# Kernel optimization log

Hardware: AMD Instinct MI355X
Metric: run time of the kernel (lower is better)

Reference implementation:

```python
import jax, jax.numpy as jnp
import numpy as np

NUM_SPECIES = 10


def setup_inputs() -> dict:
    key = jax.random.key(0)
    ks = jax.random.split(key, 8)
    n, k, d = 1024, 64, 9          # nodes, channels (num_features), irrep dim (0e+1o+2e)
    A1, A2, A3 = 3, 8, 18          # CG path counts per correlation order 1,2,3
    A = A1 + A2 + A3
    x = jax.random.normal(ks[0], (n, k, d), jnp.float32)
    counts = np.full((NUM_SPECIES,), n // NUM_SPECIES, dtype=np.int32)
    counts[0] += n - counts.sum()  # exact partition of the n nodes by species
    species_counts = jnp.asarray(counts, jnp.int32)
    w = jax.random.normal(ks[1], (NUM_SPECIES, A, k), jnp.float32) * 0.5
    projection = jax.random.normal(ks[2], (A, A), jnp.float32) / jnp.sqrt(A)
    U1 = jax.random.normal(ks[3], (d, d, A1), jnp.float32) * 0.3            # [o, i1, a]
    U2 = jax.random.normal(ks[4], (d, d, d, A2), jnp.float32) * 0.3         # [o, i1, i2, a]
    U3 = jax.random.normal(ks[5], (d, d, d, d, A3), jnp.float32) * 0.3      # [o, i1, i2, i3, a]
    return {"x": x, "species_counts": species_counts, "w": w,
            "projection": projection, "U1": U1, "U2": U2, "U3": U3}


def reference(x, species_counts, w, projection, U1, U2, U3):
    # x: [n, k, d] node features (channels k, irrep dim d)
    e = w.shape[0]
    n = x.shape[0]
    A1, A2 = U1.shape[-1], U2.shape[-1]
    # sorted per-node species index, exactly as in the original module
    species_idx = jnp.repeat(jnp.arange(e), species_counts, total_repeat_length=n)
    onehot = jax.nn.one_hot(species_idx, e, dtype=x.dtype)            # [n, e]
    # project raw weights onto the coupling-path basis: 'zau,ab->zbu'
    wp = jnp.einsum('zak,ab->zbk', w, projection)                     # [e, A, k]
    w1, w2, w3 = wp[:, :A1], wp[:, A1:A1 + A2], wp[:, A1 + A2:]
    # --- correlation 3 term, Horner scheme (MACE order) ---
    # fold species weights into the basis tensor (small: e*d^4*k)
    Uw3 = jnp.einsum('oijla,eak->eoijlk', U3, w3)                     # [e,o,i,j,l,k]
    # species-masked features (small: n*e*k*d) to avoid a per-node d^4 gather
    xe = jnp.einsum('ne,nkl->nekl', onehot, x)                        # [n,e,k,d]
    out = jnp.einsum('eoijlk,nekl->nkoij', Uw3, xe)                   # [n,k,o,i,j]
    # --- correlation 2 term ---
    c2 = jnp.einsum('oija,eak,ne->nkoij', U2, w2, onehot)             # [n,k,o,i,j]
    out = jnp.einsum('nkoij,nkj->nkoi', out + c2, x)                  # contract i2
    # --- correlation 1 term ---
    c1 = jnp.einsum('oia,eak,ne->nkoi', U1, w1, onehot)               # [n,k,o,i]
    out = jnp.einsum('nkoi,nki->nko', out + c1, x)                    # contract i1
    return out                                                        # [n, k, d_out] = n m i
```

## Files before the change

kernel.cpp:

```cpp
#include <hip/hip_runtime.h>

constexpr int N_ = 1024, K_ = 64, D_ = 9, E_ = 10;
constexpr int A1_ = 3, A2_ = 8, A3_ = 18, A_ = 29;
constexpr int NP2 = 45;
constexpr int NP3 = 165;

constexpr int OFF_WP  = 0;
constexpr int OFF_U3S = OFF_WP  + E_*A_*K_;
constexpr int OFF_U2S = OFF_U3S + NP3*D_*A3_;
constexpr int OFF_S3  = OFF_U2S + NP2*D_*A2_;
constexpr int OFF_S2  = OFF_S3  + E_*K_*NP3*D_;
constexpr int OFF_C1  = OFF_S2  + E_*K_*NP2*D_;
constexpr int WS_FLOATS = OFF_C1 + E_*K_*D_*D_;

__global__ void prep_kernel(const float* __restrict__ w,
                            const float* __restrict__ proj,
                            const float* __restrict__ U2,
                            const float* __restrict__ U3,
                            float* __restrict__ ws) {
  const int WP_N  = E_*A_*K_;
  const int U3S_N = NP3*D_*A3_;
  const int U2S_N = NP2*D_*A2_;
  int idx = blockIdx.x * blockDim.x + threadIdx.x;
  if (idx < WP_N) {
    int e = idx / (A_*K_); int r = idx % (A_*K_); int b = r / K_; int k = r % K_;
    float acc = 0.f;
    for (int a = 0; a < A_; ++a)
      acc = fmaf(w[(e*A_ + a)*K_ + k], proj[a*A_ + b], acc);
    ws[OFF_WP + idx] = acc;
  } else if (idx < WP_N + U3S_N) {
    int id = idx - WP_N;
    int t = id / (D_*A3_); int r = id % (D_*A3_); int o = r / A3_; int m = r % A3_;
    int ti = 0, tj = 0, tl = 0, c = 0;
    for (int a = 0; a < D_; ++a)
      for (int b = a; b < D_; ++b)
        for (int g = b; g < D_; ++g) { if (c == t) { ti = a; tj = b; tl = g; } ++c; }
    auto u3 = [&](int a, int b, int g) {
      return U3[(((o*D_ + a)*D_ + b)*D_ + g)*A3_ + m];
    };
    float s;
    if (ti == tj && tj == tl)      s = u3(ti, ti, ti);
    else if (ti == tj)             s = u3(ti, ti, tl) + u3(ti, tl, ti) + u3(tl, ti, ti);
    else if (tj == tl)             s = u3(ti, tj, tj) + u3(tj, ti, tj) + u3(tj, tj, ti);
    else                           s = u3(ti, tj, tl) + u3(ti, tl, tj) + u3(tj, ti, tl)
                                     + u3(tj, tl, ti) + u3(tl, ti, tj) + u3(tl, tj, ti);
    ws[OFF_U3S + id] = s;
  } else if (idx < WP_N + U3S_N + U2S_N) {
    int id = idx - WP_N - U3S_N;
    int p = id / (D_*A2_); int r = id % (D_*A2_); int o = r / A2_; int m = r % A2_;
    int pi = 0, pj = 0, c = 0;
    for (int a = 0; a < D_; ++a)
      for (int b = a; b < D_; ++b) { if (c == p) { pi = a; pj = b; } ++c; }
    float s = U2[((o*D_ + pi)*D_ + pj)*A2_ + m];
    if (pi != pj) s += U2[((o*D_ + pj)*D_ + pi)*A2_ + m];
    ws[OFF_U2S + id] = s;
  }
}

__global__ void weights_kernel(const float* __restrict__ U1,
                               float* __restrict__ ws) {
  int ek = blockIdx.x;
  int e = ek / K_, k = ek % K_;
  __shared__ float wpk[A_];
  if (threadIdx.x < A_)
    wpk[threadIdx.x] = ws[OFF_WP + (e*A_ + threadIdx.x)*K_ + k];
  __syncthreads();
  const float* u3s = ws + OFF_U3S;
  const float* u2s = ws + OFF_U2S;
  float* s3 = ws + OFF_S3 + ek*(NP3*D_);
  float* s2 = ws + OFF_S2 + ek*(NP2*D_);
  float* c1 = ws + OFF_C1 + ek*(D_*D_);
  const int TOT = NP3*D_ + NP2*D_ + D_*D_;
  for (int idx = threadIdx.x; idx < TOT; idx += blockDim.x) {
    if (idx < NP3*D_) {
      int t = idx / D_, o = idx % D_;
      float acc = 0.f;
      #pragma unroll
      for (int m = 0; m < A3_; ++m)
        acc = fmaf(u3s[(t*D_ + o)*A3_ + m], wpk[A1_ + A2_ + m], acc);
      s3[t*D_ + o] = acc;
    } else if (idx < NP3*D_ + NP2*D_) {
      int id = idx - NP3*D_;
      int p = id / D_, o = id % D_;
      float acc = 0.f;
      #pragma unroll
      for (int m = 0; m < A2_; ++m)
        acc = fmaf(u2s[(p*D_ + o)*A2_ + m], wpk[A1_ + m], acc);
      s2[p*D_ + o] = acc;
    } else {
      int id = idx - NP3*D_ - NP2*D_;
      int i = id / D_, o = id % D_;
      float acc = 0.f;
      #pragma unroll
      for (int m = 0; m < A1_; ++m)
        acc = fmaf(U1[(o*D_ + i)*A1_ + m], wpk[m], acc);
      c1[i*D_ + o] = acc;
    }
  }
}

__global__ __launch_bounds__(128) void main_kernel(const float* __restrict__ x,
                                                   const int* __restrict__ counts,
                                                   const float* __restrict__ ws,
                                                   float* __restrict__ out) {
  int ek = blockIdx.x;
  int e = ek / K_, k = ek % K_;
  int start = 0;
  for (int s = 0; s < e; ++s) start += counts[s];
  int cnt = counts[e];
  int tid = threadIdx.x;
  bool active = tid < cnt;
  int n = start + tid;
  int nc = active ? n : start;
  const float* xp = x + (nc*K_ + k)*D_;
  float xv[D_];
  #pragma unroll
  for (int l = 0; l < D_; ++l) xv[l] = xp[l];

  const float* s3 = ws + OFF_S3 + ek*(NP3*D_);
  const float* s2 = ws + OFF_S2 + ek*(NP2*D_);
  const float* c1 = ws + OFF_C1 + ek*(D_*D_);

  float acc[D_];
  #pragma unroll
  for (int o = 0; o < D_; ++o) acc[o] = 0.f;

  int t = 0, p = 0;
  #pragma unroll
  for (int i = 0; i < D_; ++i) {
    float xi = xv[i];
    #pragma unroll
    for (int o = 0; o < D_; ++o) acc[o] = fmaf(c1[i*D_ + o], xi, acc[o]);
    #pragma unroll
    for (int j = i; j < D_; ++j) {
      float xij = xi * xv[j];
      #pragma unroll
      for (int o = 0; o < D_; ++o) acc[o] = fmaf(s2[p*D_ + o], xij, acc[o]);
      ++p;
      #pragma unroll
      for (int l = j; l < D_; ++l) {
        float xijl = xij * xv[l];
        #pragma unroll
        for (int o = 0; o < D_; ++o) acc[o] = fmaf(s3[t*D_ + o], xijl, acc[o]);
        ++t;
      }
    }
  }

  if (active) {
    float* op = out + (n*K_ + k)*D_;
    #pragma unroll
    for (int o = 0; o < D_; ++o) op[o] = acc[o];
  }
}

extern "C" void kernel_launch(void* const* d_in, const int* in_sizes, int n_in,
                              void* d_out, int out_size, void* d_ws, size_t ws_size,
                              hipStream_t stream) {
  const float* x     = (const float*)d_in[0];
  const int*   cnts  = (const int*)  d_in[1];
  const float* w     = (const float*)d_in[2];
  const float* proj  = (const float*)d_in[3];
  const float* U1    = (const float*)d_in[4];
  const float* U2    = (const float*)d_in[5];
  const float* U3    = (const float*)d_in[6];
  float* out = (float*)d_out;
  float* ws  = (float*)d_ws;

  const int PREP_N = E_*A_*K_ + NP3*D_*A3_ + NP2*D_*A2_;
  int prep_blocks = (PREP_N + 255) / 256;
  prep_kernel<<<prep_blocks, 256, 0, stream>>>(w, proj, U2, U3, ws);
  weights_kernel<<<E_*K_, 256, 0, stream>>>(U1, ws);
  main_kernel<<<E_*K_, 128, 0, stream>>>(x, cnts, ws, out);
}
```

Baseline: 106.7 us.

## Fuse per-species weight folding into main kernel and transpose U tables

Merges the weights kernel into the main compute kernel, so each block first builds its own (species, channel) coefficient table into a per-block workspace slice, then runs the polynomial evaluation from it after a block barrier. The symmetrized U2/U3 tables are stored path-major so consecutive threads read consecutive addresses when folding in the weights. This removes one kernel launch and the inter-kernel dependency, at the cost of 128 threads (instead of 256) doing the table build and relying on block-level visibility of global writes.

```diff
diff --git a/kernel.cpp b/kernel.cpp
--- a/kernel.cpp
+++ b/kernel.cpp
@@ -1,17 +1,19 @@
 #include <hip/hip_runtime.h>
 
-constexpr int N_ = 1024, K_ = 64, D_ = 9, E_ = 10;
+constexpr int K_ = 64, D_ = 9, E_ = 10;
 constexpr int A1_ = 3, A2_ = 8, A3_ = 18, A_ = 29;
 constexpr int NP2 = 45;
 constexpr int NP3 = 165;
+constexpr int S3N = NP3 * D_;
+constexpr int S2N = NP2 * D_;
+constexpr int C1N = D_ * D_;
+constexpr int TBL = S3N + S2N + C1N;
 
 constexpr int OFF_WP  = 0;
 constexpr int OFF_U3S = OFF_WP  + E_*A_*K_;
-constexpr int OFF_U2S = OFF_U3S + NP3*D_*A3_;
-constexpr int OFF_S3  = OFF_U2S + NP2*D_*A2_;
-constexpr int OFF_S2  = OFF_S3  + E_*K_*NP3*D_;
-constexpr int OFF_C1  = OFF_S2  + E_*K_*NP2*D_;
-constexpr int WS_FLOATS = OFF_C1 + E_*K_*D_*D_;
+constexpr int OFF_U2S = OFF_U3S + A3_*S3N;
+constexpr int OFF_TBL = 49152;
+constexpr int SLICE   = 2048;
 
 __global__ void prep_kernel(const float* __restrict__ w,
                             const float* __restrict__ proj,
@@ -19,8 +21,8 @@
                             const float* __restrict__ U3,
                             float* __restrict__ ws) {
   const int WP_N  = E_*A_*K_;
-  const int U3S_N = NP3*D_*A3_;
-  const int U2S_N = NP2*D_*A2_;
+  const int U3S_N = A3_*S3N;
+  const int U2S_N = A2_*S2N;
   int idx = blockIdx.x * blockDim.x + threadIdx.x;
   if (idx < WP_N) {
     int e = idx / (A_*K_); int r = idx % (A_*K_); int b = r / K_; int k = r % K_;
@@ -44,7 +46,7 @@
     else if (tj == tl)             s = u3(ti, tj, tj) + u3(tj, ti, tj) + u3(tj, tj, ti);
     else                           s = u3(ti, tj, tl) + u3(ti, tl, tj) + u3(tj, ti, tl)
                                      + u3(tj, tl, ti) + u3(tl, ti, tj) + u3(tl, tj, ti);
-    ws[OFF_U3S + id] = s;
+    ws[OFF_U3S + m*S3N + t*D_ + o] = s;
   } else if (idx < WP_N + U3S_N + U2S_N) {
     int id = idx - WP_N - U3S_N;
     int p = id / (D_*A2_); int r = id % (D_*A2_); int o = r / A2_; int m = r % A2_;
@@ -53,73 +55,63 @@
       for (int b = a; b < D_; ++b) { if (c == p) { pi = a; pj = b; } ++c; }
     float s = U2[((o*D_ + pi)*D_ + pj)*A2_ + m];
     if (pi != pj) s += U2[((o*D_ + pj)*D_ + pi)*A2_ + m];
-    ws[OFF_U2S + id] = s;
+    ws[OFF_U2S + m*S2N + p*D_ + o] = s;
   }
 }
 
-__global__ void weights_kernel(const float* __restrict__ U1,
-                               float* __restrict__ ws) {
-  int ek = blockIdx.x;
-  int e = ek / K_, k = ek % K_;
-  __shared__ float wpk[A_];
-  if (threadIdx.x < A_)
-    wpk[threadIdx.x] = ws[OFF_WP + (e*A_ + threadIdx.x)*K_ + k];
+__global__ __launch_bounds__(128) void fused_kernel(
+    const float* __restrict__ x, const int* __restrict__ counts,
+    const float* __restrict__ U1, float* __restrict__ ws,
+    float* __restrict__ out) {
+  const int ek = blockIdx.x;
+  const int e = ek / K_, k = ek % K_;
+  const int tid = threadIdx.x;
+
+  __shared__ float wpk[32];
+  if (tid < A_) wpk[tid] = ws[OFF_WP + (e*A_ + tid)*K_ + k];
   __syncthreads();
+
   const float* u3s = ws + OFF_U3S;
   const float* u2s = ws + OFF_U2S;
-  float* s3 = ws + OFF_S3 + ek*(NP3*D_);
-  float* s2 = ws + OFF_S2 + ek*(NP2*D_);
-  float* c1 = ws + OFF_C1 + ek*(D_*D_);
-  const int TOT = NP3*D_ + NP2*D_ + D_*D_;
-  for (int idx = threadIdx.x; idx < TOT; idx += blockDim.x) {
-    if (idx < NP3*D_) {
-      int t = idx / D_, o = idx % D_;
-      float acc = 0.f;
+  float* g = ws + OFF_TBL + (size_t)ek * SLICE;
+
+  for (int idx = tid; idx < TBL; idx += 128) {
+    float acc = 0.f;
+    if (idx < S3N) {
       #pragma unroll
       for (int m = 0; m < A3_; ++m)
-        acc = fmaf(u3s[(t*D_ + o)*A3_ + m], wpk[A1_ + A2_ + m], acc);
-      s3[t*D_ + o] = acc;
-    } else if (idx < NP3*D_ + NP2*D_) {
-      int id = idx - NP3*D_;
-      int p = id / D_, o = id % D_;
-      float acc = 0.f;
+        acc = fmaf(u3s[m*S3N + idx], wpk[A1_ + A2_ + m], acc);
+    } else if (idx < S3N + S2N) {
+      int id = idx - S3N;
       #pragma unroll
       for (int m = 0; m < A2_; ++m)
-        acc = fmaf(u2s[(p*D_ + o)*A2_ + m], wpk[A1_ + m], acc);
-      s2[p*D_ + o] = acc;
+        acc = fmaf(u2s[m*S2N + id], wpk[A1_ + m], acc);
     } else {
-      int id = idx - NP3*D_ - NP2*D_;
+      int id = idx - S3N - S2N;
       int i = id / D_, o = id % D_;
-      float acc = 0.f;
       #pragma unroll
       for (int m = 0; m < A1_; ++m)
         acc = fmaf(U1[(o*D_ + i)*A1_ + m], wpk[m], acc);
-      c1[i*D_ + o] = acc;
     }
+    g[idx] = acc;
   }
-}
+  __syncthreads();
+  asm volatile("" ::: "memory");
 
-__global__ __launch_bounds__(128) void main_kernel(const float* __restrict__ x,
-                                                   const int* __restrict__ counts,
-                                                   const float* __restrict__ ws,
-                                                   float* __restrict__ out) {
-  int ek = blockIdx.x;
-  int e = ek / K_, k = ek % K_;
   int start = 0;
   for (int s = 0; s < e; ++s) start += counts[s];
   int cnt = counts[e];
-  int tid = threadIdx.x;
   bool active = tid < cnt;
   int n = start + tid;
   int nc = active ? n : start;
-  const float* xp = x + (nc*K_ + k)*D_;
+  const float* xp = x + (nc * K_ + k) * D_;
   float xv[D_];
   #pragma unroll
   for (int l = 0; l < D_; ++l) xv[l] = xp[l];
 
-  const float* s3 = ws + OFF_S3 + ek*(NP3*D_);
-  const float* s2 = ws + OFF_S2 + ek*(NP2*D_);
-  const float* c1 = ws + OFF_C1 + ek*(D_*D_);
+  const float* s3 = g;
+  const float* s2 = g + S3N;
+  const float* c1 = g + S3N + S2N;
 
   float acc[D_];
   #pragma unroll
@@ -130,25 +122,25 @@
   for (int i = 0; i < D_; ++i) {
     float xi = xv[i];
     #pragma unroll
-    for (int o = 0; o < D_; ++o) acc[o] = fmaf(c1[i*D_ + o], xi, acc[o]);
+    for (int o = 0; o < D_; ++o) acc[o] = fmaf(c1[i * D_ + o], xi, acc[o]);
     #pragma unroll
     for (int j = i; j < D_; ++j) {
       float xij = xi * xv[j];
       #pragma unroll
-      for (int o = 0; o < D_; ++o) acc[o] = fmaf(s2[p*D_ + o], xij, acc[o]);
+      for (int o = 0; o < D_; ++o) acc[o] = fmaf(s2[p * D_ + o], xij, acc[o]);
       ++p;
       #pragma unroll
       for (int l = j; l < D_; ++l) {
         float xijl = xij * xv[l];
         #pragma unroll
-        for (int o = 0; o < D_; ++o) acc[o] = fmaf(s3[t*D_ + o], xijl, acc[o]);
+        for (int o = 0; o < D_; ++o) acc[o] = fmaf(s3[t * D_ + o], xijl, acc[o]);
         ++t;
       }
     }
   }
 
   if (active) {
-    float* op = out + (n*K_ + k)*D_;
+    float* op = out + (n * K_ + k) * D_;
     #pragma unroll
     for (int o = 0; o < D_; ++o) op[o] = acc[o];
   }
@@ -157,19 +149,18 @@
 extern "C" void kernel_launch(void* const* d_in, const int* in_sizes, int n_in,
                               void* d_out, int out_size, void* d_ws, size_t ws_size,
                               hipStream_t stream) {
-  const float* x     = (const float*)d_in[0];
-  const int*   cnts  = (const int*)  d_in[1];
-  const float* w     = (const float*)d_in[2];
-  const float* proj  = (const float*)d_in[3];
-  const float* U1    = (const float*)d_in[4];
-  const float* U2    = (const float*)d_in[5];
-  const float* U3    = (const float*)d_in[6];
+  const float* x    = (const float*)d_in[0];
+  const int*   cnts = (const int*)  d_in[1];
+  const float* w    = (const float*)d_in[2];
+  const float* proj = (const float*)d_in[3];
+  const float* U1   = (const float*)d_in[4];
+  const float* U2   = (const float*)d_in[5];
+  const float* U3   = (const float*)d_in[6];
   float* out = (float*)d_out;
   float* ws  = (float*)d_ws;
 
-  const int PREP_N = E_*A_*K_ + NP3*D_*A3_ + NP2*D_*A2_;
+  const int PREP_N = E_*A_*K_ + A3_*S3N + A2_*S2N;
   int prep_blocks = (PREP_N + 255) / 256;
   prep_kernel<<<prep_blocks, 256, 0, stream>>>(w, proj, U2, U3, ws);
-  weights_kernel<<<E_*K_, 256, 0, stream>>>(U1, ws);
-  main_kernel<<<E_*K_, 128, 0, stream>>>(x, cnts, ws, out);
+  fused_kernel<<<E_ * K_, 128, 0, stream>>>(x, cnts, U1, ws, out);
 }
```

Measured after the change: 364.5 us. +241.7%, slower.
